# Performance work log

Measured on AMD Instinct MI355X. Metric: run time of the kernel, lower is better.

The kernel has to match this reference:

```python
import jax, jax.numpy as jnp
import numpy as np

HIDDEN = 1024

def _cat_linear(x, W, b, cat_ids):
    # x: (B,T,Din), W: (C,Din,Dout), b: (C,Dout)
    return jnp.einsum('bti,bio->bto', x, W[cat_ids]) + b[cat_ids][:, None, :]

def _sinusoidal(timesteps, dim):
    # timesteps: (B,T) int -> (B,T,dim)
    t = timesteps.astype(jnp.float32)
    half = dim // 2
    exponent = -jnp.arange(half, dtype=jnp.float32) * (jnp.log(10000.0) / half)
    freqs = t[..., None] * jnp.exp(exponent)
    return jnp.concatenate([jnp.sin(freqs), jnp.cos(freqs)], axis=-1)

def setup_inputs() -> dict:
    key = jax.random.key(0)
    ks = jax.random.split(key, 8)
    B, T, A, H, C = 64, 64, 64, HIDDEN, 16
    actions = jax.random.normal(ks[0], (B, T, A), dtype=jnp.float32)
    timesteps = jax.random.randint(ks[1], (B,), 0, 1000)
    cat_ids = jax.random.randint(ks[2], (B,), 0, C)
    W1 = 0.02 * jax.random.normal(ks[3], (C, A, H), dtype=jnp.float32)
    b1 = jnp.zeros((C, H), dtype=jnp.float32)
    W2 = 0.02 * jax.random.normal(ks[4], (C, 2 * H, H), dtype=jnp.float32)
    b2 = jnp.zeros((C, H), dtype=jnp.float32)
    W3 = 0.02 * jax.random.normal(ks[5], (C, H, H), dtype=jnp.float32)
    b3 = jnp.zeros((C, H), dtype=jnp.float32)
    return {"actions": actions, "timesteps": timesteps, "cat_ids": cat_ids,
            "W1": W1, "b1": b1, "W2": W2, "b2": b2, "W3": W3, "b3": b3}

def reference(actions, timesteps, cat_ids, W1, b1, W2, b2, W3, b3):
    B, T, _ = actions.shape
    ts = jnp.broadcast_to(timesteps[:, None], (B, T))  # (B,T)
    a_emb = _cat_linear(actions, W1, b1, cat_ids)        # (B,T,H)
    tau = _sinusoidal(ts, HIDDEN).astype(a_emb.dtype)    # (B,T,H)
    x = jnp.concatenate([a_emb, tau], axis=-1)           # (B,T,2H)
    h = _cat_linear(x, W2, b2, cat_ids)
    h = h * jax.nn.sigmoid(h)                            # swish
    return _cat_linear(h, W3, b3, cat_ids)               # (B,T,H)
```

## Files before the change

### kernel.cpp

```cpp
#include <hip/hip_runtime.h>
#include <hip/hip_bf16.h>
#include <math.h>


typedef short bf16x8 __attribute__((ext_vector_type(8)));
typedef float floatx4 __attribute__((ext_vector_type(4)));

__device__ inline short f2bf(float f) {
  union { float f; unsigned u; } v; v.f = f;
  unsigned u = v.u;
  unsigned r = (u + 0x7fffu + ((u >> 16) & 1u)) >> 16;
  return (short)(r & 0xffffu);
}

template<int K, bool A_F32, bool SWISH, bool OUT_BF16>
__global__ __launch_bounds__(256) void gemm_kernel(
    const void* __restrict__ Aall, int lda,
    const float* __restrict__ Wall,
    const float* __restrict__ bias,
    const int* __restrict__ cat_ids,
    void* __restrict__ Out, int ldo)
{
  constexpr int N = 1024;
  const int b    = blockIdx.y;
  const int c    = cat_ids[b];
  const int tid  = threadIdx.x;
  const int wave = tid >> 6;
  const int lane = tid & 63;
  const int quad = lane >> 4;
  const int l16  = lane & 15;
  const int n_wave = blockIdx.x * 128 + wave * 32;

  const float* W  = Wall + (size_t)c * K * N;
  const float* bs = bias + (size_t)c * N;

  floatx4 acc[4][2];
  #pragma unroll
  for (int mt = 0; mt < 4; ++mt)
    #pragma unroll
    for (int nt = 0; nt < 2; ++nt)
      acc[mt][nt] = (floatx4){0.f, 0.f, 0.f, 0.f};

  const float* Af = (const float*)Aall + (size_t)(b * 64) * lda;
  const short* Ab = (const short*)Aall + (size_t)(b * 64) * lda;

  #pragma unroll 2
  for (int k0 = 0; k0 < K; k0 += 32) {
    const int kk = k0 + quad * 8;

    bf16x8 af[4];
    #pragma unroll
    for (int mt = 0; mt < 4; ++mt) {
      const int row = mt * 16 + l16;
      if constexpr (A_F32) {
        const floatx4* p = (const floatx4*)(Af + (size_t)row * lda + kk);
        floatx4 x0 = p[0];
        floatx4 x1 = p[1];
        bf16x8 t;
        t[0] = f2bf(x0[0]); t[1] = f2bf(x0[1]); t[2] = f2bf(x0[2]); t[3] = f2bf(x0[3]);
        t[4] = f2bf(x1[0]); t[5] = f2bf(x1[1]); t[6] = f2bf(x1[2]); t[7] = f2bf(x1[3]);
        af[mt] = t;
      } else {
        af[mt] = *(const bf16x8*)(Ab + (size_t)row * lda + kk);
      }
    }

    bf16x8 bfr[2];
    #pragma unroll
    for (int nt = 0; nt < 2; ++nt) {
      const int n = n_wave + nt * 16 + l16;
      const float* wp = W + (size_t)kk * N + n;
      bf16x8 t;
      #pragma unroll
      for (int j = 0; j < 8; ++j) t[j] = f2bf(wp[(size_t)j * N]);
      bfr[nt] = t;
    }

    #pragma unroll
    for (int nt = 0; nt < 2; ++nt)
      #pragma unroll
      for (int mt = 0; mt < 4; ++mt)
        acc[mt][nt] = __builtin_amdgcn_mfma_f32_16x16x32_bf16(af[mt], bfr[nt], acc[mt][nt], 0, 0, 0);
  }

  #pragma unroll
  for (int nt = 0; nt < 2; ++nt) {
    const int n = n_wave + nt * 16 + l16;
    const float bv = bs[n];
    #pragma unroll
    for (int mt = 0; mt < 4; ++mt) {
      #pragma unroll
      for (int r = 0; r < 4; ++r) {
        const int row = mt * 16 + quad * 4 + r;
        float v = acc[mt][nt][r] + bv;
        if constexpr (SWISH) v = v / (1.f + __expf(-v));
        if constexpr (OUT_BF16)
          ((short*)Out)[(size_t)(b * 64 + row) * ldo + n] = f2bf(v);
        else
          ((float*)Out)[(size_t)(b * 64 + row) * ldo + n] = v;
      }
    }
  }
}

__global__ __launch_bounds__(256) void tau_kernel(const int* __restrict__ ts,
                                                  short* __restrict__ x)
{
  const int b = blockIdx.x;
  const float t = (float)ts[b];
  const int tid = threadIdx.x;
  #pragma unroll
  for (int q = 0; q < 4; ++q) {
    const int i  = q * 256 + tid;
    const int hi = i & 511;
    const float e = __expf(-(float)hi * 0.017988946039015980f);
    const float freq = t * e;
    const float v = (i < 512) ? sinf(freq) : cosf(freq);
    const short sv = f2bf(v);
    short* base = x + (size_t)(b * 64) * 2048 + 1024 + i;
    #pragma unroll 4
    for (int tt = 0; tt < 64; ++tt) base[(size_t)tt * 2048] = sv;
  }
}

extern "C" void kernel_launch(void* const* d_in, const int* in_sizes, int n_in,
                              void* d_out, int out_size, void* d_ws, size_t ws_size,
                              hipStream_t stream) {
  const float* actions   = (const float*)d_in[0];
  const int*   timesteps = (const int*)  d_in[1];
  const int*   cat_ids   = (const int*)  d_in[2];
  const float* W1 = (const float*)d_in[3];
  const float* b1 = (const float*)d_in[4];
  const float* W2 = (const float*)d_in[5];
  const float* b2 = (const float*)d_in[6];
  const float* W3 = (const float*)d_in[7];
  const float* b3 = (const float*)d_in[8];

  short* x = (short*)d_ws;
  short* h = x + (size_t)64 * 64 * 2048;

  dim3 grid(8, 64), blk(256);

  gemm_kernel<64, true, false, true><<<grid, blk, 0, stream>>>(
      (const void*)actions, 64, W1, b1, cat_ids, (void*)x, 2048);

  tau_kernel<<<64, 256, 0, stream>>>(timesteps, x);

  gemm_kernel<2048, false, true, true><<<grid, blk, 0, stream>>>(
      (const void*)x, 2048, W2, b2, cat_ids, (void*)h, 1024);

  gemm_kernel<1024, false, false, false><<<grid, blk, 0, stream>>>(
      (const void*)h, 1024, W3, b3, cat_ids, d_out, 1024);
}
```

Baseline: 400.2 us.

## Sort batches by category and pair them per block to share weight tiles

```diff
diff --git a/kernel.cpp b/kernel.cpp
--- a/kernel.cpp
+++ b/kernel.cpp
@@ -13,6 +13,14 @@
   return (short)(r & 0xffffu);
 }
 
+__device__ inline bf16x8 loadB(const float* __restrict__ wp) {
+  constexpr int N = 1024;
+  bf16x8 t;
+  #pragma unroll
+  for (int j = 0; j < 8; ++j) t[j] = f2bf(wp[(size_t)j * N]);
+  return t;
+}
+
 template<int K, bool A_F32, bool SWISH, bool OUT_BF16>
 __global__ __launch_bounds__(256) void gemm_kernel(
     const void* __restrict__ Aall, int lda,
@@ -22,83 +30,93 @@
     void* __restrict__ Out, int ldo)
 {
   constexpr int N = 1024;
-  const int b    = blockIdx.y;
-  const int c    = cat_ids[b];
-  const int tid  = threadIdx.x;
+  __shared__ int s_b[64], s_c[64];
+
+  const int tid = threadIdx.x;
+  if (tid < 64) {
+    const int myc = cat_ids[tid];
+    int pos = 0;
+    #pragma unroll
+    for (int c = 0; c < 16; ++c) {
+      unsigned long long m = __ballot(myc == c);
+      if (c < myc)       pos += __popcll(m);
+      else if (c == myc) pos += __popcll(m & ((1ull << tid) - 1ull));
+    }
+    s_b[pos] = tid;
+    s_c[pos] = myc;
+  }
+  __syncthreads();
+
+  const int e  = blockIdx.y;
+  const int b0 = s_b[2 * e],     b1 = s_b[2 * e + 1];
+  const int c0 = s_c[2 * e],     c1 = s_c[2 * e + 1];
+  const bool same = (c0 == c1);
+
   const int wave = tid >> 6;
   const int lane = tid & 63;
   const int quad = lane >> 4;
   const int l16  = lane & 15;
-  const int n_wave = blockIdx.x * 128 + wave * 32;
+  const int n    = blockIdx.x * 64 + wave * 16 + l16;
 
-  const float* W  = Wall + (size_t)c * K * N;
-  const float* bs = bias + (size_t)c * N;
+  const float* W0 = Wall + (size_t)c0 * K * N;
+  const float* W1 = Wall + (size_t)c1 * K * N;
 
-  floatx4 acc[4][2];
+  const char* arow[8];
   #pragma unroll
-  for (int mt = 0; mt < 4; ++mt)
-    #pragma unroll
-    for (int nt = 0; nt < 2; ++nt)
-      acc[mt][nt] = (floatx4){0.f, 0.f, 0.f, 0.f};
+  for (int mt = 0; mt < 8; ++mt) {
+    const int row = ((mt < 4) ? b0 : b1) * 64 + (mt & 3) * 16 + l16;
+    arow[mt] = (const char*)Aall + (size_t)row * lda * (A_F32 ? 4 : 2);
+  }
 
-  const float* Af = (const float*)Aall + (size_t)(b * 64) * lda;
-  const short* Ab = (const short*)Aall + (size_t)(b * 64) * lda;
+  floatx4 acc[8];
+  #pragma unroll
+  for (int mt = 0; mt < 8; ++mt) acc[mt] = (floatx4){0.f, 0.f, 0.f, 0.f};
 
   #pragma unroll 2
   for (int k0 = 0; k0 < K; k0 += 32) {
     const int kk = k0 + quad * 8;
 
-    bf16x8 af[4];
+    bf16x8 bf0 = loadB(W0 + (size_t)kk * N + n);
+    bf16x8 bf1;
+    if (same) bf1 = bf0;
+    else      bf1 = loadB(W1 + (size_t)kk * N + n);
+
+    bf16x8 af[8];
     #pragma unroll
-    for (int mt = 0; mt < 4; ++mt) {
-      const int row = mt * 16 + l16;
+    for (int mt = 0; mt < 8; ++mt) {
       if constexpr (A_F32) {
-        const floatx4* p = (const floatx4*)(Af + (size_t)row * lda + kk);
-        floatx4 x0 = p[0];
-        floatx4 x1 = p[1];
+        const floatx4* p = (const floatx4*)(arow[mt] + (size_t)kk * 4);
+        floatx4 x0 = p[0], x1 = p[1];
         bf16x8 t;
         t[0] = f2bf(x0[0]); t[1] = f2bf(x0[1]); t[2] = f2bf(x0[2]); t[3] = f2bf(x0[3]);
         t[4] = f2bf(x1[0]); t[5] = f2bf(x1[1]); t[6] = f2bf(x1[2]); t[7] = f2bf(x1[3]);
         af[mt] = t;
       } else {
-        af[mt] = *(const bf16x8*)(Ab + (size_t)row * lda + kk);
+        af[mt] = *(const bf16x8*)(arow[mt] + (size_t)kk * 2);
       }
     }
 
-    bf16x8 bfr[2];
     #pragma unroll
-    for (int nt = 0; nt < 2; ++nt) {
-      const int n = n_wave + nt * 16 + l16;
-      const float* wp = W + (size_t)kk * N + n;
-      bf16x8 t;
-      #pragma unroll
-      for (int j = 0; j < 8; ++j) t[j] = f2bf(wp[(size_t)j * N]);
-      bfr[nt] = t;
-    }
-
-    #pragma unroll
-    for (int nt = 0; nt < 2; ++nt)
-      #pragma unroll
-      for (int mt = 0; mt < 4; ++mt)
-        acc[mt][nt] = __builtin_amdgcn_mfma_f32_16x16x32_bf16(af[mt], bfr[nt], acc[mt][nt], 0, 0, 0);
+    for (int mt = 0; mt < 8; ++mt)
+      acc[mt] = __builtin_amdgcn_mfma_f32_16x16x32_bf16(
+          af[mt], (mt < 4) ? bf0 : bf1, acc[mt], 0, 0, 0);
   }
 
+  const float bv0 = bias[(size_t)c0 * N + n];
+  const float bv1 = bias[(size_t)c1 * N + n];
   #pragma unroll
-  for (int nt = 0; nt < 2; ++nt) {
-    const int n = n_wave + nt * 16 + l16;
-    const float bv = bs[n];
+  for (int mt = 0; mt < 8; ++mt) {
+    const int bb = (mt < 4) ? b0 : b1;
+    const float bv = (mt < 4) ? bv0 : bv1;
     #pragma unroll
-    for (int mt = 0; mt < 4; ++mt) {
-      #pragma unroll
-      for (int r = 0; r < 4; ++r) {
-        const int row = mt * 16 + quad * 4 + r;
-        float v = acc[mt][nt][r] + bv;
-        if constexpr (SWISH) v = v / (1.f + __expf(-v));
-        if constexpr (OUT_BF16)
-          ((short*)Out)[(size_t)(b * 64 + row) * ldo + n] = f2bf(v);
-        else
-          ((float*)Out)[(size_t)(b * 64 + row) * ldo + n] = v;
-      }
+    for (int r = 0; r < 4; ++r) {
+      const int row = bb * 64 + (mt & 3) * 16 + quad * 4 + r;
+      float v = acc[mt][r] + bv;
+      if constexpr (SWISH) v = v / (1.f + __expf(-v));
+      if constexpr (OUT_BF16)
+        ((short*)Out)[(size_t)row * ldo + n] = f2bf(v);
+      else
+        ((float*)Out)[(size_t)row * ldo + n] = v;
     }
   }
 }
@@ -139,7 +157,7 @@
   short* x = (short*)d_ws;
   short* h = x + (size_t)64 * 64 * 2048;
 
-  dim3 grid(8, 64), blk(256);
+  dim3 grid(16, 32), blk(256);
 
   gemm_kernel<64, true, false, true><<<grid, blk, 0, stream>>>(
       (const void*)actions, 64, W1, b1, cat_ids, (void*)x, 2048);
```

New measurement: 468.0 us. 16.9% more time.

## Group batches by category pairs and stage weight tiles in LDS with double buffering

Applied to the files above, without the earlier changes.

```diff
diff --git a/kernel.cpp b/kernel.cpp
--- a/kernel.cpp
+++ b/kernel.cpp
@@ -9,8 +9,68 @@
 __device__ inline short f2bf(float f) {
   union { float f; unsigned u; } v; v.f = f;
   unsigned u = v.u;
-  unsigned r = (u + 0x7fffu + ((u >> 16) & 1u)) >> 16;
-  return (short)(r & 0xffffu);
+  return (short)(((u + 0x7fffu + ((u >> 16) & 1u)) >> 16) & 0xffffu);
+}
+
+__device__ inline unsigned pk2(float a, float b) {
+  union { float f; unsigned u; } x, y; x.f = a; y.f = b;
+  unsigned ua = (x.u + 0x7fffu + ((x.u >> 16) & 1u)) >> 16;
+  unsigned ub = (y.u + 0x7fffu + ((y.u >> 16) & 1u)) >> 16;
+  return (ua & 0xffffu) | (ub << 16);
+}
+
+#if __has_builtin(__builtin_amdgcn_global_load_lds)
+__device__ inline void async16(float* lds, const float* g) {
+  __builtin_amdgcn_global_load_lds(
+      (const __attribute__((address_space(1))) unsigned int*)g,
+      (__attribute__((address_space(3))) unsigned int*)lds, 16, 0, 0);
+}
+#define ASYNC_LDS 1
+#else
+__device__ inline void async16(float* lds, const float* g) {
+  *(floatx4*)lds = *(const floatx4*)g;
+}
+#define ASYNC_LDS 0
+#endif
+
+__device__ inline void stage_tile(float* tilebuf, const float* __restrict__ Wsrc,
+                                  int tid) {
+  const int wave = tid >> 6;
+#if ASYNC_LDS
+  #pragma unroll
+  for (int i = 0; i < 4; ++i) {
+    const int s  = i * 256 + tid;
+    const int k  = s >> 5;
+    const int p  = s & 31;
+    const int cc = (p - 4 * (k >> 3)) & 31;
+    const float* g = Wsrc + (size_t)k * 1024 + cc * 4;
+    float* l = tilebuf + (size_t)(i * 256 + wave * 64) * 4;
+    async16(l, g);
+  }
+#else
+  #pragma unroll
+  for (int i = 0; i < 4; ++i) {
+    const int s  = i * 256 + tid;
+    const int k  = s >> 5;
+    const int p  = s & 31;
+    const int cc = (p - 4 * (k >> 3)) & 31;
+    *(floatx4*)(tilebuf + (size_t)s * 4) =
+        *(const floatx4*)(Wsrc + (size_t)k * 1024 + cc * 4);
+  }
+#endif
+}
+
+__device__ inline bf16x8 read_bfrag(const float* __restrict__ tile, int col, int quad) {
+  const int cc = col >> 2, c3 = col & 3;
+  const int p  = (cc + 4 * quad) & 31;
+  const float* base = tile + (size_t)p * 4 + c3 + (size_t)(quad * 8) * 128;
+  float f[8];
+  #pragma unroll
+  for (int j = 0; j < 8; ++j) f[j] = base[(size_t)j * 128];
+  union { bf16x8 v; unsigned u[4]; } r;
+  #pragma unroll
+  for (int j = 0; j < 4; ++j) r.u[j] = pk2(f[2 * j], f[2 * j + 1]);
+  return r.v;
 }
 
 template<int K, bool A_F32, bool SWISH, bool OUT_BF16>
@@ -21,83 +81,118 @@
     const int* __restrict__ cat_ids,
     void* __restrict__ Out, int ldo)
 {
-  constexpr int N = 1024;
-  const int b    = blockIdx.y;
-  const int c    = cat_ids[b];
-  const int tid  = threadIdx.x;
-  const int wave = tid >> 6;
-  const int lane = tid & 63;
-  const int quad = lane >> 4;
-  const int l16  = lane & 15;
-  const int n_wave = blockIdx.x * 128 + wave * 32;
-
-  const float* W  = Wall + (size_t)c * K * N;
-  const float* bs = bias + (size_t)c * N;
-
-  floatx4 acc[4][2];
+  constexpr int N  = 1024;
+  constexpr int KT = K / 32;
+  __shared__ float wtile[2][32 * 128];
+  __shared__ int s_b[80], s_c[80], s_np;
+
+  const int tid = threadIdx.x;
+  if (tid < 80) { s_b[tid] = -1; s_c[tid] = 0; }
+  __syncthreads();
+  if (tid < 64) {
+    const int myc = cat_ids[tid];
+    int rank = 0, pst = 0, tot = 0;
+    #pragma unroll
+    for (int c = 0; c < 16; ++c) {
+      unsigned long long m = __ballot(myc == c);
+      const int cnt = __popcll(m);
+      const int pc  = 2 * ((cnt + 1) >> 1);
+      if (c < myc)  pst += pc;
+      if (c == myc) rank = __popcll(m & ((1ull << tid) - 1ull));
+      tot += pc;
+    }
+    const int slot = pst + rank;
+    s_b[slot] = tid;
+    s_c[slot] = myc;
+    if (tid == 0) s_np = tot >> 1;
+  }
+  __syncthreads();
+
+  const int e = blockIdx.y;
+  if (e >= s_np) return;
+  const int b0v = s_b[2 * e];
+  int b1 = s_b[2 * e + 1];
+  const int c = s_c[2 * e];
+  const bool st1 = (b1 >= 0);
+  if (!st1) b1 = b0v;
+
+  const int wave = tid >> 6, lane = tid & 63;
+  const int quad = lane >> 4, l16 = lane & 15;
+  const int wm = wave >> 1, wn = wave & 1;
+  const int ns = blockIdx.x * 128;
+  const float* Wc = Wall + (size_t)c * K * N + ns;
+
+  const char* arow[4];
+  #pragma unroll
+  for (int mt = 0; mt < 4; ++mt) {
+    const int pr = wm * 64 + mt * 16 + l16;
+    const int batch = (pr < 64) ? b0v : b1;
+    const int row = batch * 64 + (pr & 63);
+    arow[mt] = (const char*)Aall + (size_t)row * lda * (A_F32 ? 4 : 2);
+  }
+
+  floatx4 acc[4][4];
   #pragma unroll
   for (int mt = 0; mt < 4; ++mt)
     #pragma unroll
-    for (int nt = 0; nt < 2; ++nt)
+    for (int nt = 0; nt < 4; ++nt)
       acc[mt][nt] = (floatx4){0.f, 0.f, 0.f, 0.f};
 
-  const float* Af = (const float*)Aall + (size_t)(b * 64) * lda;
-  const short* Ab = (const short*)Aall + (size_t)(b * 64) * lda;
-
-  #pragma unroll 2
-  for (int k0 = 0; k0 < K; k0 += 32) {
-    const int kk = k0 + quad * 8;
+  stage_tile(&wtile[0][0], Wc, tid);
+  int buf = 0;
+  for (int kt = 0; kt < KT; ++kt) {
+    __syncthreads();
+    if (kt + 1 < KT)
+      stage_tile(&wtile[buf ^ 1][0], Wc + (size_t)(kt + 1) * 32 * 1024, tid);
+
+    const float* tp = &wtile[buf][0];
+    const int kk = kt * 32 + quad * 8;
 
     bf16x8 af[4];
     #pragma unroll
     for (int mt = 0; mt < 4; ++mt) {
-      const int row = mt * 16 + l16;
       if constexpr (A_F32) {
-        const floatx4* p = (const floatx4*)(Af + (size_t)row * lda + kk);
-        floatx4 x0 = p[0];
-        floatx4 x1 = p[1];
-        bf16x8 t;
-        t[0] = f2bf(x0[0]); t[1] = f2bf(x0[1]); t[2] = f2bf(x0[2]); t[3] = f2bf(x0[3]);
-        t[4] = f2bf(x1[0]); t[5] = f2bf(x1[1]); t[6] = f2bf(x1[2]); t[7] = f2bf(x1[3]);
-        af[mt] = t;
+        const floatx4* p = (const floatx4*)(arow[mt] + (size_t)kk * 4);
+        floatx4 x0 = p[0], x1 = p[1];
+        union { bf16x8 v; unsigned u[4]; } t;
+        t.u[0] = pk2(x0[0], x0[1]); t.u[1] = pk2(x0[2], x0[3]);
+        t.u[2] = pk2(x1[0], x1[1]); t.u[3] = pk2(x1[2], x1[3]);
+        af[mt] = t.v;
       } else {
-        af[mt] = *(const bf16x8*)(Ab + (size_t)row * lda + kk);
+        af[mt] = *(const bf16x8*)(arow[mt] + (size_t)kk * 2);
       }
     }
 
-    bf16x8 bfr[2];
-    #pragma unroll
-    for (int nt = 0; nt < 2; ++nt) {
-      const int n = n_wave + nt * 16 + l16;
-      const float* wp = W + (size_t)kk * N + n;
-      bf16x8 t;
-      #pragma unroll
-      for (int j = 0; j < 8; ++j) t[j] = f2bf(wp[(size_t)j * N]);
-      bfr[nt] = t;
-    }
-
-    #pragma unroll
-    for (int nt = 0; nt < 2; ++nt)
+    #pragma unroll
+    for (int nt = 0; nt < 4; ++nt) {
+      bf16x8 bf = read_bfrag(tp, wn * 64 + nt * 16 + l16, quad);
       #pragma unroll
       for (int mt = 0; mt < 4; ++mt)
-        acc[mt][nt] = __builtin_amdgcn_mfma_f32_16x16x32_bf16(af[mt], bfr[nt], acc[mt][nt], 0, 0, 0);
-  }
-
-  #pragma unroll
-  for (int nt = 0; nt < 2; ++nt) {
-    const int n = n_wave + nt * 16 + l16;
-    const float bv = bs[n];
+        acc[mt][nt] = __builtin_amdgcn_mfma_f32_16x16x32_bf16(af[mt], bf, acc[mt][nt], 0, 0, 0);
+    }
+    buf ^= 1;
+  }
+
+  #pragma unroll
+  for (int nt = 0; nt < 4; ++nt) {
+    const int col = ns + wn * 64 + nt * 16 + l16;
+    const float bv = bias[(size_t)c * N + col];
     #pragma unroll
     for (int mt = 0; mt < 4; ++mt) {
+      const int prb = wm * 64 + mt * 16 + quad * 4;
+      const int batch = (prb < 64) ? b0v : b1;
+      const bool do_store = (prb < 64) || st1;
       #pragma unroll
       for (int r = 0; r < 4; ++r) {
-        const int row = mt * 16 + quad * 4 + r;
+        const int row = batch * 64 + ((prb + r) & 63);
         float v = acc[mt][nt][r] + bv;
         if constexpr (SWISH) v = v / (1.f + __expf(-v));
-        if constexpr (OUT_BF16)
-          ((short*)Out)[(size_t)(b * 64 + row) * ldo + n] = f2bf(v);
-        else
-          ((float*)Out)[(size_t)(b * 64 + row) * ldo + n] = v;
+        if (do_store) {
+          if constexpr (OUT_BF16)
+            ((short*)Out)[(size_t)row * ldo + col] = f2bf(v);
+          else
+            ((float*)Out)[(size_t)row * ldo + col] = v;
+        }
       }
     }
   }
@@ -139,7 +234,7 @@
   short* x = (short*)d_ws;
   short* h = x + (size_t)64 * 64 * 2048;
 
-  dim3 grid(8, 64), blk(256);
+  dim3 grid(8, 40), blk(256);
 
   gemm_kernel<64, true, false, true><<<grid, blk, 0, stream>>>(
       (const void*)actions, 64, W1, b1, cat_ids, (void*)x, 2048);
```

New measurement: 376.4 us. -5.9%, faster.
